# Performance work log

Hardware: AMD Instinct MI355X
Metric: run time of the kernel (lower is better)

## Reference

```python
import jax, jax.numpy as jnp
import numpy as np

N_NODES = 100000
N_EDGES = 600000
IN_C, HID, OUT_C = 128, 256, 1

def _glorot(key, shape):
    fan_in, fan_out = shape[1], shape[0]
    lim = np.sqrt(6.0 / (fan_in + fan_out))
    return jax.random.uniform(key, shape, jnp.float32, -lim, lim)

def setup_inputs() -> dict:
    key = jax.random.key(0)
    ks = jax.random.split(key, 12)
    x = jax.random.normal(ks[0], (N_NODES, IN_C), jnp.float32)
    edge_index = jax.random.randint(ks[1], (2, N_EDGES), 0, N_NODES, jnp.int32)
    return {
        "x": x,
        "edge_index": edge_index,
        # SAGEConv1: lin_l (neighbors, with bias), lin_r (root, no bias)
        "W1l": _glorot(ks[2], (HID, IN_C)),
        "b1": jnp.zeros((HID,), jnp.float32),
        "W1r": _glorot(ks[3], (HID, IN_C)),
        # SAGEConv2
        "W2l": _glorot(ks[4], (HID, HID)),
        "b2": jnp.zeros((HID,), jnp.float32),
        "W2r": _glorot(ks[5], (HID, HID)),
        # MLP head: Linear(HID, HID//2) -> ReLU -> Linear(HID//2, OUT_C)
        "Wf1": _glorot(ks[6], (HID // 2, HID)),
        "bf1": jnp.zeros((HID // 2,), jnp.float32),
        "Wf2": _glorot(ks[7], (OUT_C, HID // 2)),
        "bf2": jnp.zeros((OUT_C,), jnp.float32),
    }

def _sage_conv(x, src, dst, Wl, b, Wr, n_nodes):
    # mean-aggregate source-node features into destination nodes
    msgs = x[src]  # [E, F] gather
    sums = jax.ops.segment_sum(msgs, dst, num_segments=n_nodes)
    cnt = jax.ops.segment_sum(jnp.ones((src.shape[0], 1), x.dtype), dst,
                              num_segments=n_nodes)
    mean = sums / jnp.maximum(cnt, 1.0)  # isolated nodes -> 0
    return mean @ Wl.T + b + x @ Wr.T

def reference(x, edge_index, W1l, b1, W1r, W2l, b2, W2r, Wf1, bf1, Wf2, bf2):
    src, dst = edge_index[0], edge_index[1]
    n = x.shape[0]
    h = jax.nn.elu(_sage_conv(x, src, dst, W1l, b1, W1r, n))
    # dropout p=0.3 is identity in eval mode
    h = jax.nn.elu(_sage_conv(h, src, dst, W2l, b2, W2r, n))
    h = jax.nn.relu(h @ Wf1.T + bf1)
    out = h @ Wf2.T + bf2  # [N, 1]
    return jnp.squeeze(out)
```

## Files before the change

kernel.cpp:

```cpp
#include <hip/hip_runtime.h>
#include <hip/hip_bf16.h>

#define NN 100000
#define NE 600000
#define NBLK 98
#define MPAD 100096

typedef __attribute__((ext_vector_type(4))) int   i32x4;
typedef __attribute__((ext_vector_type(4))) float f32x4;

__device__ __forceinline__ float b2f(unsigned short u) {
  unsigned int v = ((unsigned int)u) << 16;
  return __uint_as_float(v);
}
__device__ __forceinline__ unsigned short f2b(float f) {
  __hip_bfloat16 h = __float2bfloat16(f);
  return *reinterpret_cast<unsigned short*>(&h);
}
__device__ __forceinline__ float elu(float v) {
  return v > 0.0f ? v : (expf(v) - 1.0f);
}
__device__ __forceinline__ void gload_lds16(const void* g, void* l) {
  __builtin_amdgcn_global_load_lds(
      (const __attribute__((address_space(1))) void*)g,
      (__attribute__((address_space(3))) void*)l, 16, 0, 0);
}
__device__ __forceinline__ f32x4 mfma16(i32x4 a, i32x4 b, f32x4 c) {
  asm volatile("v_mfma_f32_16x16x32_bf16 %0, %1, %2, %0"
               : "+v"(c) : "v"(a), "v"(b));
  return c;
}
#define WAITV0() asm volatile("s_waitcnt vmcnt(0)" ::: "memory")
#define BAR() asm volatile("s_barrier" ::: "memory")

__global__ __launch_bounds__(256) void hist_kernel(
    const int* __restrict__ ei, int* __restrict__ deg) {
  const int* dst = ei + NE;
  int i = blockIdx.x * 256 + threadIdx.x;
  int n = gridDim.x * 256;
  for (int e = i; e < NE; e += n) atomicAdd(&deg[dst[e]], 1);
}

__global__ __launch_bounds__(256) void scan1_kernel(
    const int* __restrict__ deg, int* __restrict__ row, int* __restrict__ aux) {
  __shared__ int sd[256];
  int b = blockIdx.x, t = threadIdx.x;
  int base = b * 1024 + t * 4;
  int v0 = (base + 0 < NN) ? deg[base + 0] : 0;
  int v1 = (base + 1 < NN) ? deg[base + 1] : 0;
  int v2 = (base + 2 < NN) ? deg[base + 2] : 0;
  int v3 = (base + 3 < NN) ? deg[base + 3] : 0;
  int s = v0 + v1 + v2 + v3;
  sd[t] = s;
  __syncthreads();
  for (int off = 1; off < 256; off <<= 1) {
    int tmp = (t >= off) ? sd[t - off] : 0;
    __syncthreads();
    sd[t] += tmp;
    __syncthreads();
  }
  int excl = sd[t] - s;
  if (base + 0 < NN) row[base + 0] = excl;
  if (base + 1 < NN) row[base + 1] = excl + v0;
  if (base + 2 < NN) row[base + 2] = excl + v0 + v1;
  if (base + 3 < NN) row[base + 3] = excl + v0 + v1 + v2;
  if (t == 255) aux[b] = sd[t];
}

__global__ __launch_bounds__(256) void scan2_kernel(int* __restrict__ aux) {
  __shared__ int sd[256];
  int t = threadIdx.x;
  int v = (t < NBLK) ? aux[t] : 0;
  sd[t] = v;
  __syncthreads();
  for (int off = 1; off < 256; off <<= 1) {
    int tmp = (t >= off) ? sd[t - off] : 0;
    __syncthreads();
    sd[t] += tmp;
    __syncthreads();
  }
  if (t < NBLK) aux[t] = sd[t] - v;
}

__global__ __launch_bounds__(256) void scan3_kernel(
    int* __restrict__ row, const int* __restrict__ aux) {
  int i = blockIdx.x * 256 + threadIdx.x;
  if (i < NN) row[i] += aux[i >> 10];
  if (i == 0) row[NN] = NE;
}

__global__ __launch_bounds__(256) void fill_kernel(
    const int* __restrict__ ei, const int* __restrict__ row,
    int* __restrict__ cur, int* __restrict__ eidx) {
  const int* src = ei;
  const int* dst = ei + NE;
  int i = blockIdx.x * 256 + threadIdx.x;
  int n = gridDim.x * 256;
  for (int e = i; e < NE; e += n) {
    int d = dst[e];
    int p = atomicAdd(&cur[d], 1);
    eidx[row[d] + p] = src[e];
  }
}

__global__ __launch_bounds__(256) void conv_x(
    const float* __restrict__ x, unsigned short* __restrict__ A1) {
  int i = blockIdx.x * 256 + threadIdx.x;
  if (i >= NN * 32) return;
  int n = i >> 5, k4 = i & 31;
  float4 v = ((const float4*)(x + (size_t)n * 128))[k4];
  ushort4 o;
  o.x = f2b(v.x); o.y = f2b(v.y); o.z = f2b(v.z); o.w = f2b(v.w);
  ((ushort4*)(A1 + (size_t)n * 256 + 128))[k4] = o;
}

__global__ __launch_bounds__(256) void conv_w(
    const float* __restrict__ W1l, const float* __restrict__ W1r,
    const float* __restrict__ W2l, const float* __restrict__ W2r,
    const float* __restrict__ Wf1,
    unsigned short* __restrict__ W1b, unsigned short* __restrict__ W2b,
    unsigned short* __restrict__ Wf1b) {
  int i = blockIdx.x * 256 + threadIdx.x;
  const float* srcp;
  unsigned short* dstp;
  if (i < 16384) {
    int e = i * 4, j = e >> 8, k = e & 255;
    srcp = (k < 128) ? (W1l + (size_t)j * 128 + k) : (W1r + (size_t)j * 128 + (k - 128));
    dstp = W1b + e;
  } else if (i < 49152) {
    int e = (i - 16384) * 4, j = e >> 9, k = e & 511;
    srcp = (k < 256) ? (W2l + (size_t)j * 256 + k) : (W2r + (size_t)j * 256 + (k - 256));
    dstp = W2b + e;
  } else if (i < 57344) {
    int e = (i - 49152) * 4;
    srcp = Wf1 + e;
    dstp = Wf1b + e;
  } else return;
  float4 v = *(const float4*)srcp;
  ushort4 o;
  o.x = f2b(v.x); o.y = f2b(v.y); o.z = f2b(v.z); o.w = f2b(v.w);
  *(ushort4*)dstp = o;
}

__global__ __launch_bounds__(256) void agg1_csr(
    unsigned short* __restrict__ A1, const int* __restrict__ row,
    const int* __restrict__ eidx) {
  int lane = threadIdx.x & 63;
  int n = (blockIdx.x * 256 + threadIdx.x) >> 6;
  if (n >= NN) return;
  int r0 = row[n], r1 = row[n + 1];
  float ax = 0.f, ay = 0.f;
  int e = r0;
  for (; e + 3 < r1; e += 4) {
    int s0 = eidx[e], s1 = eidx[e + 1], s2 = eidx[e + 2], s3 = eidx[e + 3];
    ushort2 a = ((const ushort2*)(A1 + (size_t)s0 * 256 + 128))[lane];
    ushort2 b = ((const ushort2*)(A1 + (size_t)s1 * 256 + 128))[lane];
    ushort2 c = ((const ushort2*)(A1 + (size_t)s2 * 256 + 128))[lane];
    ushort2 d = ((const ushort2*)(A1 + (size_t)s3 * 256 + 128))[lane];
    ax += (b2f(a.x) + b2f(b.x)) + (b2f(c.x) + b2f(d.x));
    ay += (b2f(a.y) + b2f(b.y)) + (b2f(c.y) + b2f(d.y));
  }
  for (; e < r1; ++e) {
    int s0 = eidx[e];
    ushort2 a = ((const ushort2*)(A1 + (size_t)s0 * 256 + 128))[lane];
    ax += b2f(a.x);
    ay += b2f(a.y);
  }
  float inv = 1.0f / (float)max(r1 - r0, 1);
  ushort2 o;
  o.x = f2b(ax * inv);
  o.y = f2b(ay * inv);
  ((ushort2*)(A1 + (size_t)n * 256))[lane] = o;
}

__global__ __launch_bounds__(256) void agg2_csr(
    unsigned short* __restrict__ A2, const int* __restrict__ row,
    const int* __restrict__ eidx) {
  int lane = threadIdx.x & 63;
  int n = (blockIdx.x * 256 + threadIdx.x) >> 6;
  if (n >= NN) return;
  int r0 = row[n], r1 = row[n + 1];
  float4 acc = make_float4(0.f, 0.f, 0.f, 0.f);
  int e = r0;
  for (; e + 3 < r1; e += 4) {
    int s0 = eidx[e], s1 = eidx[e + 1], s2 = eidx[e + 2], s3 = eidx[e + 3];
    ushort4 a = ((const ushort4*)(A2 + (size_t)s0 * 512 + 256))[lane];
    ushort4 b = ((const ushort4*)(A2 + (size_t)s1 * 512 + 256))[lane];
    ushort4 c = ((const ushort4*)(A2 + (size_t)s2 * 512 + 256))[lane];
    ushort4 d = ((const ushort4*)(A2 + (size_t)s3 * 512 + 256))[lane];
    acc.x += (b2f(a.x) + b2f(b.x)) + (b2f(c.x) + b2f(d.x));
    acc.y += (b2f(a.y) + b2f(b.y)) + (b2f(c.y) + b2f(d.y));
    acc.z += (b2f(a.z) + b2f(b.z)) + (b2f(c.z) + b2f(d.z));
    acc.w += (b2f(a.w) + b2f(b.w)) + (b2f(c.w) + b2f(d.w));
  }
  for (; e < r1; ++e) {
    int s0 = eidx[e];
    ushort4 a = ((const ushort4*)(A2 + (size_t)s0 * 512 + 256))[lane];
    acc.x += b2f(a.x);
    acc.y += b2f(a.y);
    acc.z += b2f(a.z);
    acc.w += b2f(a.w);
  }
  float inv = 1.0f / (float)max(r1 - r0, 1);
  ushort4 o;
  o.x = f2b(acc.x * inv);
  o.y = f2b(acc.y * inv);
  o.z = f2b(acc.z * inv);
  o.w = f2b(acc.w * inv);
  ((ushort4*)(A2 + (size_t)n * 512))[lane] = o;
}

template <int K, int APITCH, int NF, int EPI>
__global__ __launch_bounds__(256, 2) void gemm_kernel(
    const unsigned short* __restrict__ A, const unsigned short* __restrict__ Wb,
    const float* __restrict__ bias, const float* __restrict__ w2,
    const float* __restrict__ bf2p,
    unsigned short* __restrict__ Hout, int HPITCH, int HOFF,
    float* __restrict__ out) {
  __shared__ unsigned short lA[2][4096];
  __shared__ unsigned short lB[2][NF * 512];
  int tid = threadIdx.x;
  int w = tid >> 6, lane = tid & 63;
  int lhi = lane >> 4, llo = lane & 15;
  int m0 = blockIdx.x * 128;
  int fb = lane * 8;

  f32x4 acc0[NF], acc1[NF];
#pragma unroll
  for (int n = 0; n < NF; ++n) { acc0[n] = (f32x4)0.f; acc1[n] = (f32x4)0.f; }

#define STAGE(t)                                                                \
  do {                                                                          \
    int _b = (t) & 1;                                                           \
    int _k0 = (t) * 32;                                                         \
    _Pragma("unroll")                                                           \
    for (int i = 0; i < 2; ++i) {                                               \
      int c = w * 2 + i;                                                        \
      const unsigned short* ga =                                                \
          A + (size_t)(m0 + c * 16 + llo) * APITCH + _k0 + lhi * 8;             \
      gload_lds16(ga, &lA[_b][c * 512]);                                        \
    }                                                                           \
    _Pragma("unroll")                                                           \
    for (int i = 0; i < NF / 4; ++i) {                                          \
      int c = w * (NF / 4) + i;                                                 \
      const unsigned short* gb =                                                \
          Wb + (size_t)(c * 16 + llo) * K + _k0 + lhi * 8;                      \
      gload_lds16(gb, &lB[_b][c * 512]);                                        \
    }                                                                           \
  } while (0)

  constexpr int NSTEP = K / 32;
  STAGE(0);
  for (int t = 0; t < NSTEP; ++t) {
    WAITV0();
    BAR();
    if (t + 1 < NSTEP) STAGE(t + 1);
    const unsigned short* la = &lA[t & 1][0];
    const unsigned short* lb = &lB[t & 1][0];
    i32x4 a0 = *(const i32x4*)(la + (w * 2 + 0) * 512 + fb);
    i32x4 a1 = *(const i32x4*)(la + (w * 2 + 1) * 512 + fb);
#pragma unroll
    for (int n = 0; n < NF; ++n) {
      i32x4 b = *(const i32x4*)(lb + n * 512 + fb);
      acc0[n] = mfma16(a0, b, acc0[n]);
      acc1[n] = mfma16(a1, b, acc1[n]);
    }
  }
#undef STAGE
  asm volatile("s_nop 7\n\ts_nop 7");

  if constexpr (EPI == 0) {
    float bv[NF];
#pragma unroll
    for (int n = 0; n < NF; ++n) bv[n] = bias[n * 16 + llo];
#pragma unroll
    for (int mi = 0; mi < 2; ++mi) {
#pragma unroll
      for (int n = 0; n < NF; ++n) {
        f32x4 av = mi ? acc1[n] : acc0[n];
#pragma unroll
        for (int r = 0; r < 4; ++r) {
          int R = m0 + (w * 2 + mi) * 16 + lhi * 4 + r;
          float v = elu(av[r] + bv[n]);
          Hout[(size_t)R * HPITCH + HOFF + n * 16 + llo] = f2b(v);
        }
      }
    }
  } else {
    float b1v[NF], w2v[NF];
#pragma unroll
    for (int n = 0; n < NF; ++n) {
      b1v[n] = bias[n * 16 + llo];
      w2v[n] = w2[n * 16 + llo];
    }
    float bf2v = bf2p[0];
#pragma unroll
    for (int mi = 0; mi < 2; ++mi) {
#pragma unroll
      for (int r = 0; r < 4; ++r) {
        float s = 0.f;
#pragma unroll
        for (int n = 0; n < NF; ++n) {
          f32x4 av = mi ? acc1[n] : acc0[n];
          s += fmaxf(av[r] + b1v[n], 0.f) * w2v[n];
        }
        s += __shfl_xor(s, 1);
        s += __shfl_xor(s, 2);
        s += __shfl_xor(s, 4);
        s += __shfl_xor(s, 8);
        int R = m0 + (w * 2 + mi) * 16 + lhi * 4 + r;
        if (llo == 0 && R < NN) out[R] = s + bf2v;
      }
    }
  }
}

extern "C" void kernel_launch(void* const* d_in, const int* in_sizes, int n_in,
                              void* d_out, int out_size, void* d_ws, size_t ws_size,
                              hipStream_t stream) {
  const float* x   = (const float*)d_in[0];
  const int*   ei  = (const int*)d_in[1];
  const float* W1l = (const float*)d_in[2];
  const float* b1  = (const float*)d_in[3];
  const float* W1r = (const float*)d_in[4];
  const float* W2l = (const float*)d_in[5];
  const float* b2  = (const float*)d_in[6];
  const float* W2r = (const float*)d_in[7];
  const float* Wf1 = (const float*)d_in[8];
  const float* bf1 = (const float*)d_in[9];
  const float* Wf2 = (const float*)d_in[10];
  const float* bf2 = (const float*)d_in[11];
  float* out = (float*)d_out;

  char* ws = (char*)d_ws;
  size_t o = 0;
  int* deg = (int*)(ws + o); o += 400384;
  int* cur = (int*)(ws + o); o += 400384;
  size_t zero_bytes = o;
  int* row  = (int*)(ws + o); o += 400640;
  int* aux  = (int*)(ws + o); o += 4096;
  int* eidx = (int*)(ws + o); o += 2400000;
  unsigned short* A1 = (unsigned short*)(ws + o); o += (size_t)MPAD * 256 * 2;
  unsigned short* A2 = (unsigned short*)(ws + o); o += (size_t)MPAD * 512 * 2;
  unsigned short* h2 = (unsigned short*)(ws + o); o += (size_t)MPAD * 256 * 2;
  unsigned short* W1b  = (unsigned short*)(ws + o); o += 131072;
  unsigned short* W2b  = (unsigned short*)(ws + o); o += 262144;
  unsigned short* Wf1b = (unsigned short*)(ws + o); o += 65536;

  hipMemsetAsync(d_ws, 0, zero_bytes, stream);

  hist_kernel<<<2048, 256, 0, stream>>>(ei, deg);
  scan1_kernel<<<NBLK, 256, 0, stream>>>(deg, row, aux);
  scan2_kernel<<<1, 256, 0, stream>>>(aux);
  scan3_kernel<<<(NN + 255) / 256, 256, 0, stream>>>(row, aux);
  fill_kernel<<<2048, 256, 0, stream>>>(ei, row, cur, eidx);

  conv_x<<<(NN * 32 + 255) / 256, 256, 0, stream>>>(x, A1);
  conv_w<<<224, 256, 0, stream>>>(W1l, W1r, W2l, W2r, Wf1, W1b, W2b, Wf1b);

  agg1_csr<<<25000, 256, 0, stream>>>(A1, row, eidx);
  gemm_kernel<256, 256, 16, 0><<<MPAD / 128, 256, 0, stream>>>(
      A1, W1b, b1, nullptr, nullptr, A2, 512, 256, nullptr);
  agg2_csr<<<25000, 256, 0, stream>>>(A2, row, eidx);
  gemm_kernel<512, 512, 16, 0><<<MPAD / 128, 256, 0, stream>>>(
      A2, W2b, b2, nullptr, nullptr, h2, 256, 0, nullptr);
  gemm_kernel<256, 256, 8, 1><<<MPAD / 128, 256, 0, stream>>>(
      h2, Wf1b, bf1, Wf2, bf2, nullptr, 0, 0, out);
}
```

Baseline: 327.1 us.

## Load GEMM operands directly from global memory and split output columns across grid

The GEMM kernel no longer stages A and B tiles through LDS with double buffering and barriers. Each wave now reads its MFMA fragments straight from global memory, relying on cache for reuse. The two hidden-layer GEMMs split the 256 output columns over a second grid dimension (NF 16 to 8), and the occupancy hint rises to 3 blocks per CU. This removes barrier and LDS overhead and doubles block count, at the cost of redundant global/L2 traffic and uncoalesced, cache-dependent loads.

```diff
diff --git a/kernel.cpp b/kernel.cpp
--- a/kernel.cpp
+++ b/kernel.cpp
@@ -20,18 +20,11 @@
 __device__ __forceinline__ float elu(float v) {
   return v > 0.0f ? v : (expf(v) - 1.0f);
 }
-__device__ __forceinline__ void gload_lds16(const void* g, void* l) {
-  __builtin_amdgcn_global_load_lds(
-      (const __attribute__((address_space(1))) void*)g,
-      (__attribute__((address_space(3))) void*)l, 16, 0, 0);
-}
 __device__ __forceinline__ f32x4 mfma16(i32x4 a, i32x4 b, f32x4 c) {
   asm volatile("v_mfma_f32_16x16x32_bf16 %0, %1, %2, %0"
                : "+v"(c) : "v"(a), "v"(b));
   return c;
 }
-#define WAITV0() asm volatile("s_waitcnt vmcnt(0)" ::: "memory")
-#define BAR() asm volatile("s_barrier" ::: "memory")
 
 __global__ __launch_bounds__(256) void hist_kernel(
     const int* __restrict__ ei, int* __restrict__ deg) {
@@ -211,68 +204,45 @@
 }
 
 template <int K, int APITCH, int NF, int EPI>
-__global__ __launch_bounds__(256, 2) void gemm_kernel(
+__global__ __launch_bounds__(256, 3) void gemm_kernel(
     const unsigned short* __restrict__ A, const unsigned short* __restrict__ Wb,
     const float* __restrict__ bias, const float* __restrict__ w2,
     const float* __restrict__ bf2p,
     unsigned short* __restrict__ Hout, int HPITCH, int HOFF,
     float* __restrict__ out) {
-  __shared__ unsigned short lA[2][4096];
-  __shared__ unsigned short lB[2][NF * 512];
   int tid = threadIdx.x;
   int w = tid >> 6, lane = tid & 63;
   int lhi = lane >> 4, llo = lane & 15;
   int m0 = blockIdx.x * 128;
-  int fb = lane * 8;
+  int c0 = blockIdx.y * (NF * 16);
 
   f32x4 acc0[NF], acc1[NF];
 #pragma unroll
   for (int n = 0; n < NF; ++n) { acc0[n] = (f32x4)0.f; acc1[n] = (f32x4)0.f; }
 
-#define STAGE(t)                                                                \
-  do {                                                                          \
-    int _b = (t) & 1;                                                           \
-    int _k0 = (t) * 32;                                                         \
-    _Pragma("unroll")                                                           \
-    for (int i = 0; i < 2; ++i) {                                               \
-      int c = w * 2 + i;                                                        \
-      const unsigned short* ga =                                                \
-          A + (size_t)(m0 + c * 16 + llo) * APITCH + _k0 + lhi * 8;             \
-      gload_lds16(ga, &lA[_b][c * 512]);                                        \
-    }                                                                           \
-    _Pragma("unroll")                                                           \
-    for (int i = 0; i < NF / 4; ++i) {                                          \
-      int c = w * (NF / 4) + i;                                                 \
-      const unsigned short* gb =                                                \
-          Wb + (size_t)(c * 16 + llo) * K + _k0 + lhi * 8;                      \
-      gload_lds16(gb, &lB[_b][c * 512]);                                        \
-    }                                                                           \
-  } while (0)
+  const unsigned short* pa0 = A + (size_t)(m0 + w * 32 + llo) * APITCH + lhi * 8;
+  const unsigned short* pa1 = pa0 + (size_t)16 * APITCH;
+  const unsigned short* pb  = Wb + (size_t)(c0 + llo) * K + lhi * 8;
 
   constexpr int NSTEP = K / 32;
-  STAGE(0);
+#pragma unroll 2
   for (int t = 0; t < NSTEP; ++t) {
-    WAITV0();
-    BAR();
-    if (t + 1 < NSTEP) STAGE(t + 1);
-    const unsigned short* la = &lA[t & 1][0];
-    const unsigned short* lb = &lB[t & 1][0];
-    i32x4 a0 = *(const i32x4*)(la + (w * 2 + 0) * 512 + fb);
-    i32x4 a1 = *(const i32x4*)(la + (w * 2 + 1) * 512 + fb);
+    int ko = t * 32;
+    i32x4 a0 = *(const i32x4*)(pa0 + ko);
+    i32x4 a1 = *(const i32x4*)(pa1 + ko);
 #pragma unroll
     for (int n = 0; n < NF; ++n) {
-      i32x4 b = *(const i32x4*)(lb + n * 512 + fb);
+      i32x4 b = *(const i32x4*)(pb + (size_t)n * 16 * K + ko);
       acc0[n] = mfma16(a0, b, acc0[n]);
       acc1[n] = mfma16(a1, b, acc1[n]);
     }
   }
-#undef STAGE
   asm volatile("s_nop 7\n\ts_nop 7");
 
   if constexpr (EPI == 0) {
     float bv[NF];
 #pragma unroll
-    for (int n = 0; n < NF; ++n) bv[n] = bias[n * 16 + llo];
+    for (int n = 0; n < NF; ++n) bv[n] = bias[c0 + n * 16 + llo];
 #pragma unroll
     for (int mi = 0; mi < 2; ++mi) {
 #pragma unroll
@@ -282,7 +252,7 @@
         for (int r = 0; r < 4; ++r) {
           int R = m0 + (w * 2 + mi) * 16 + lhi * 4 + r;
           float v = elu(av[r] + bv[n]);
-          Hout[(size_t)R * HPITCH + HOFF + n * 16 + llo] = f2b(v);
+          Hout[(size_t)R * HPITCH + HOFF + c0 + n * 16 + llo] = f2b(v);
         }
       }
     }
@@ -359,11 +329,11 @@
   conv_w<<<224, 256, 0, stream>>>(W1l, W1r, W2l, W2r, Wf1, W1b, W2b, Wf1b);
 
   agg1_csr<<<25000, 256, 0, stream>>>(A1, row, eidx);
-  gemm_kernel<256, 256, 16, 0><<<MPAD / 128, 256, 0, stream>>>(
+  gemm_kernel<256, 256, 8, 0><<<dim3(MPAD / 128, 2), 256, 0, stream>>>(
       A1, W1b, b1, nullptr, nullptr, A2, 512, 256, nullptr);
   agg2_csr<<<25000, 256, 0, stream>>>(A2, row, eidx);
-  gemm_kernel<512, 512, 16, 0><<<MPAD / 128, 256, 0, stream>>>(
+  gemm_kernel<512, 512, 8, 0><<<dim3(MPAD / 128, 2), 256, 0, stream>>>(
       A2, W2b, b2, nullptr, nullptr, h2, 256, 0, nullptr);
-  gemm_kernel<256, 256, 8, 1><<<MPAD / 128, 256, 0, stream>>>(
+  gemm_kernel<256, 256, 8, 1><<<dim3(MPAD / 128, 1), 256, 0, stream>>>(
       h2, Wf1b, bf1, Wf2, bf2, nullptr, 0, 0, out);
 }
```

Result: slower. 434.8 us (+32.9%).
